# Optimization experiments

Measured on AMD Instinct MI355X. Metric: run time of the kernel, lower is better.

The kernel has to match this reference:

```python
import jax, jax.numpy as jnp
import numpy as np


def setup_inputs() -> dict:
    key = jax.random.key(0)
    k1, k2 = jax.random.split(key)
    B, T, C = 32, 1024, 384
    MAX_LEN = 8192
    x = jax.random.normal(k1, (B, T, C), dtype=jnp.float32)
    duration = jax.random.randint(k2, (B, T), 0, 8, dtype=jnp.int64)
    return {"x": x, "duration": duration, "max_len": MAX_LEN}


def reference(x, duration, max_len):
    # x: [B, T, C] float; duration: [B, T] int frame counts; max_len: python int.
    # Equivalent of per-row repeat_interleave(x, duration) followed by zero-pad
    # to max_len, done as one fused cumsum + searchsorted + gather.
    B, T, C = x.shape
    cum = jnp.cumsum(duration, axis=1)            # [B, T] end frame of each phoneme
    mel_len = cum[:, -1]                          # [B] total expanded length
    pos = jnp.arange(max_len)                     # [max_len] output frame indices
    # For output frame j, source phoneme = first i with cum[i] > j
    idx = jax.vmap(lambda c: jnp.searchsorted(c, pos, side="right"))(cum)  # [B, max_len]
    idx = jnp.minimum(idx, T - 1)
    mask = pos[None, :] < mel_len[:, None]        # [B, max_len] valid (non-pad) frames
    out = jnp.take_along_axis(x, idx[:, :, None], axis=1)  # [B, max_len, C]
    out = jnp.where(mask[:, :, None], out, jnp.zeros((), dtype=x.dtype))
    return out, mel_len
```

## Files before the change

### kernel.cpp

```cpp
#include <hip/hip_runtime.h>


#define BB 32
#define TT 1024
#define CC 384
#define MAXLEN 8192
#define OUT0 (BB * MAXLEN * CC)
#define NT 512
#define ROWS_PER_BLK 256
#define NCHUNK (MAXLEN / ROWS_PER_BLK)
#define QPR (CC / 4)
#define QPB (ROWS_PER_BLK * QPR)
#define ITERS (QPB / NT)

typedef float f32x4 __attribute__((ext_vector_type(4)));

__global__ __launch_bounds__(NT) void lr_fused(const int* __restrict__ dur,
                                               const f32x4* __restrict__ x4,
                                               f32x4* __restrict__ out4,
                                               float* __restrict__ mel_out) {
    __shared__ int sd[TT];
    __shared__ int ss[NT];
    __shared__ int sidx[ROWS_PER_BLK];
    const int b     = blockIdx.y;
    const int chunk = blockIdx.x;
    const int t     = threadIdx.x;

    sd[t]      = dur[b * TT + t];
    sd[t + NT] = dur[b * TT + t + NT];
    __syncthreads();
    ss[t] = sd[2 * t] + sd[2 * t + 1];
    __syncthreads();
    #pragma unroll
    for (int off = 1; off < NT; off <<= 1) {
        int v = (t >= off) ? ss[t - off] : 0;
        __syncthreads();
        ss[t] += v;
        __syncthreads();
    }
    int inc = ss[t];
    int d1  = sd[2 * t + 1];
    __syncthreads();
    sd[2 * t + 1] = inc;
    sd[2 * t]     = inc - d1;
    __syncthreads();
    const int ml = sd[TT - 1];
    if (chunk == 0 && t == 0) mel_out[b] = (float)ml;

    if (t < ROWS_PER_BLK) {
        int p = chunk * ROWS_PER_BLK + t;
        int r = -1;
        if (p < ml) {
            int lo = 0, hi = TT;
            while (lo < hi) {
                int mid = (lo + hi) >> 1;
                if (sd[mid] <= p) lo = mid + 1; else hi = mid;
            }
            r = (lo < TT - 1) ? lo : (TT - 1);
        }
        sidx[t] = r;
    }
    __syncthreads();

    const f32x4* __restrict__ xb = x4 + (size_t)b * TT * QPR;
    f32x4* __restrict__ ob = out4 + (size_t)(b * MAXLEN + chunk * ROWS_PER_BLK) * QPR;
    #pragma unroll 4
    for (int k = 0; k < ITERS; ++k) {
        unsigned q    = (unsigned)t + (unsigned)k * NT;
        unsigned row  = q / QPR;
        unsigned lane = q - row * QPR;
        int i = sidx[row];
        f32x4 v = (f32x4)0.f;
        if (i >= 0) v = xb[(unsigned)i * QPR + lane];
        __builtin_nontemporal_store(v, &ob[q]);
    }
}

extern "C" void kernel_launch(void* const* d_in, const int* in_sizes, int n_in,
                              void* d_out, int out_size, void* d_ws, size_t ws_size,
                              hipStream_t stream) {
    const float* x   = (const float*)d_in[0];
    const int*   dur = (const int*)d_in[1];
    float* out = (float*)d_out;

    dim3 grid(NCHUNK, BB);
    lr_fused<<<grid, NT, 0, stream>>>(dur, (const f32x4*)x, (f32x4*)out, out + OUT0);
}
```

Baseline: 90.80 us.

## Replace LDS Hillis-Steele scan with wavefront shuffle scan and halve block size

The per-block cumulative sum over durations is rebuilt: each thread loads an int4, does a local serial scan, then uses a shuffle-based wavefront scan plus a small cross-wave sum instead of the many-barrier shared-memory scan. Blocks are also halved to 256 threads and 128 output rows, doubling the grid to 2048 blocks. This is meant to cut barrier and LDS overhead in the scan prologue and improve load balance. The cost is that the scan is now recomputed by twice as many blocks.

```diff
diff --git a/kernel.cpp b/kernel.cpp
--- a/kernel.cpp
+++ b/kernel.cpp
@@ -6,55 +6,60 @@
 #define CC 384
 #define MAXLEN 8192
 #define OUT0 (BB * MAXLEN * CC)
-#define NT 512
-#define ROWS_PER_BLK 256
-#define NCHUNK (MAXLEN / ROWS_PER_BLK)
+#define NT 256
+#define ROWS 128
 #define QPR (CC / 4)
-#define QPB (ROWS_PER_BLK * QPR)
-#define ITERS (QPB / NT)
+#define ITERS (ROWS * QPR / NT)
 
 typedef float f32x4 __attribute__((ext_vector_type(4)));
 
-__global__ __launch_bounds__(NT) void lr_fused(const int* __restrict__ dur,
+__global__ __launch_bounds__(NT) void lr_fused(const int4* __restrict__ dur4,
                                                const f32x4* __restrict__ x4,
                                                f32x4* __restrict__ out4,
                                                float* __restrict__ mel_out) {
-    __shared__ int sd[TT];
-    __shared__ int ss[NT];
-    __shared__ int sidx[ROWS_PER_BLK];
-    const int b     = blockIdx.y;
-    const int chunk = blockIdx.x;
+    __shared__ int cum[TT];
+    __shared__ int sidx[ROWS];
+    __shared__ int wsum[NT / 64];
+    const int bid   = blockIdx.x;
+    const int b     = bid >> 6;
+    const int chunk = bid & 63;
     const int t     = threadIdx.x;
+    const int lane  = t & 63;
+    const int w     = t >> 6;
 
-    sd[t]      = dur[b * TT + t];
-    sd[t + NT] = dur[b * TT + t + NT];
+    int4 d = dur4[b * (TT / 4) + t];
+    int s0 = d.x;
+    int s1 = s0 + d.y;
+    int s2 = s1 + d.z;
+    int s3 = s2 + d.w;
+    int v = s3;
+    #pragma unroll
+    for (int dd = 1; dd < 64; dd <<= 1) {
+        int u = __shfl_up(v, dd);
+        if (lane >= dd) v += u;
+    }
+    if (lane == 63) wsum[w] = v;
     __syncthreads();
-    ss[t] = sd[2 * t] + sd[2 * t + 1];
+    int prefix = 0;
+    #pragma unroll
+    for (int i = 0; i < NT / 64; ++i) prefix += (i < w) ? wsum[i] : 0;
+    const int base = prefix + v - s3;
+    cum[4 * t + 0] = base + s0;
+    cum[4 * t + 1] = base + s1;
+    cum[4 * t + 2] = base + s2;
+    cum[4 * t + 3] = base + s3;
     __syncthreads();
-    #pragma unroll
-    for (int off = 1; off < NT; off <<= 1) {
-        int v = (t >= off) ? ss[t - off] : 0;
-        __syncthreads();
-        ss[t] += v;
-        __syncthreads();
-    }
-    int inc = ss[t];
-    int d1  = sd[2 * t + 1];
-    __syncthreads();
-    sd[2 * t + 1] = inc;
-    sd[2 * t]     = inc - d1;
-    __syncthreads();
-    const int ml = sd[TT - 1];
+    const int ml = cum[TT - 1];
     if (chunk == 0 && t == 0) mel_out[b] = (float)ml;
 
-    if (t < ROWS_PER_BLK) {
-        int p = chunk * ROWS_PER_BLK + t;
+    if (t < ROWS) {
+        int p = chunk * ROWS + t;
         int r = -1;
         if (p < ml) {
             int lo = 0, hi = TT;
             while (lo < hi) {
                 int mid = (lo + hi) >> 1;
-                if (sd[mid] <= p) lo = mid + 1; else hi = mid;
+                if (cum[mid] <= p) lo = mid + 1; else hi = mid;
             }
             r = (lo < TT - 1) ? lo : (TT - 1);
         }
@@ -63,16 +68,16 @@
     __syncthreads();
 
     const f32x4* __restrict__ xb = x4 + (size_t)b * TT * QPR;
-    f32x4* __restrict__ ob = out4 + (size_t)(b * MAXLEN + chunk * ROWS_PER_BLK) * QPR;
+    f32x4* __restrict__ ob = out4 + ((size_t)b * MAXLEN + (size_t)chunk * ROWS) * QPR;
     #pragma unroll 4
     for (int k = 0; k < ITERS; ++k) {
         unsigned q    = (unsigned)t + (unsigned)k * NT;
         unsigned row  = q / QPR;
-        unsigned lane = q - row * QPR;
+        unsigned ln   = q - row * QPR;
         int i = sidx[row];
-        f32x4 v = (f32x4)0.f;
-        if (i >= 0) v = xb[(unsigned)i * QPR + lane];
-        __builtin_nontemporal_store(v, &ob[q]);
+        f32x4 vv = (f32x4)0.f;
+        if (i >= 0) vv = xb[(unsigned)i * QPR + ln];
+        __builtin_nontemporal_store(vv, &ob[q]);
     }
 }
 
@@ -83,6 +88,6 @@
     const int*   dur = (const int*)d_in[1];
     float* out = (float*)d_out;
 
-    dim3 grid(NCHUNK, BB);
-    lr_fused<<<grid, NT, 0, stream>>>(dur, (const f32x4*)x, (f32x4*)out, out + OUT0);
+    lr_fused<<<BB * 64, NT, 0, stream>>>((const int4*)dur, (const f32x4*)x,
+                                         (f32x4*)out, out + OUT0);
 }
```

After: 90.34 us. About the same (-0.5%).
